# Performance work log

Hardware: AMD Instinct MI355X
Metric: run time of the kernel (lower is better)

The kernel has to match this reference:

```python
import jax, jax.numpy as jnp
import numpy as np

B, Q, K = 4, 512, 512
QUERY_SIZE = 512
KEY_SIZE = 512
NUM_HIDDENS = 256


def setup_inputs() -> dict:
    key = jax.random.key(0)
    k1, k2, k3, k4, k5 = jax.random.split(key, 5)
    queries = jax.random.normal(k1, (B, Q, 1, QUERY_SIZE), dtype=jnp.float32)
    keys = jax.random.normal(k2, (B, 1, K, KEY_SIZE), dtype=jnp.float32)
    # nn.Linear weights (bias=False); stored as (in, out) for einsum clarity
    W_q = jax.random.normal(k3, (QUERY_SIZE, NUM_HIDDENS), dtype=jnp.float32) * (1.0 / np.sqrt(QUERY_SIZE))
    W_k = jax.random.normal(k4, (KEY_SIZE, NUM_HIDDENS), dtype=jnp.float32) * (1.0 / np.sqrt(KEY_SIZE))
    w_v = jax.random.normal(k5, (NUM_HIDDENS,), dtype=jnp.float32) * (1.0 / np.sqrt(NUM_HIDDENS))
    return {"queries": queries, "keys": keys, "W_q": W_q, "W_k": W_k, "w_v": w_v}


def reference(queries, keys, W_q, W_k, w_v):
    # Project: queries (B,Q,1,Dq) -> (B,Q,1,H); keys (B,1,K,Dk) -> (B,1,K,H)
    q = jnp.einsum('bqod,dh->bqoh', queries, W_q)
    k = jnp.einsum('bokd,dh->bokh', keys, W_k)
    # Broadcast add -> (B,Q,K,H), tanh, reduce hidden via w_v -> (B,Q,K)
    features = jnp.tanh(q + k)
    scores = jnp.einsum('bqkh,h->bqk', features, w_v)
    return scores
```

## Files before the change

### kernel.cpp

```cpp
#include <hip/hip_runtime.h>
#include <hip/hip_bf16.h>

#define HH 256
#define DD 512
#define MM 2048
#define CSCALE 2.8853900817779268f

typedef __bf16 bf16x8 __attribute__((ext_vector_type(8)));
typedef float floatx4 __attribute__((ext_vector_type(4)));

__global__ __launch_bounds__(256) void prep_kernel(
    const float* __restrict__ Wq, const float* __restrict__ Wk,
    const float* __restrict__ wv,
    __bf16* __restrict__ Wt, float* __restrict__ wv2, float* __restrict__ sumWp)
{
  const int bx = blockIdx.x;
  if (bx < 256) {
    const int mat  = bx >> 7;
    const int tile = bx & 127;
    const int kt = tile & 15;
    const int nt = tile >> 4;
    const float* __restrict__ W = mat ? Wk : Wq;
    __bf16* __restrict__ Wo = Wt + (size_t)mat * HH * DD;
    __shared__ float lds[32][33];
    const int i = threadIdx.x >> 5;
    const int j = threadIdx.x & 31;
    const int k0 = kt * 32, n0 = nt * 32;
#pragma unroll
    for (int p = 0; p < 4; ++p)
      lds[i + p * 8][j] = W[(k0 + i + p * 8) * HH + n0 + j];
    __syncthreads();
#pragma unroll
    for (int p = 0; p < 4; ++p) {
      const int n = i + p * 8;
      Wo[(n0 + n) * DD + k0 + j] = (__bf16)(lds[j][n] * CSCALE);
    }
  } else {
    __shared__ float red[256];
    const int t = threadIdx.x;
    float w = wv[t];
    wv2[t] = -2.0f * w;
    red[t] = w;
    __syncthreads();
    for (int s = 128; s > 0; s >>= 1) {
      if (t < s) red[t] += red[t + s];
      __syncthreads();
    }
    if (t == 0) *sumWp = red[0];
  }
}

__global__ __launch_bounds__(256) void proj_kernel(
    const float* __restrict__ queries, const float* __restrict__ keys,
    const __bf16* __restrict__ Wt,
    __bf16* __restrict__ eqp, float* __restrict__ ekp)
{
  const int w    = threadIdx.x >> 6;
  const int lane = threadIdx.x & 63;
  const int quad = lane >> 4;
  const int r    = lane & 15;
  const bool is_k = (blockIdx.z != 0);
  const float* __restrict__ X = is_k ? keys : queries;
  const __bf16* __restrict__ Wb = Wt + (is_k ? (size_t)HH * DD : 0);

  const int m0 = blockIdx.x * 32 + (w >> 1) * 16;
  const int n0 = blockIdx.y * 64 + (w & 1) * 32;

  floatx4 acc0 = {0.f, 0.f, 0.f, 0.f};
  floatx4 acc1 = {0.f, 0.f, 0.f, 0.f};
  const float* arow = X + (size_t)(m0 + r) * DD + quad * 8;
  const __bf16* b0 = Wb + (size_t)(n0 + r) * DD + quad * 8;
  const __bf16* b1 = b0 + 16 * DD;

  for (int kk = 0; kk < DD; kk += 32) {
    float4 a0 = *(const float4*)(arow + kk);
    float4 a1 = *(const float4*)(arow + kk + 4);
    bf16x8 af;
    af[0] = (__bf16)a0.x; af[1] = (__bf16)a0.y;
    af[2] = (__bf16)a0.z; af[3] = (__bf16)a0.w;
    af[4] = (__bf16)a1.x; af[5] = (__bf16)a1.y;
    af[6] = (__bf16)a1.z; af[7] = (__bf16)a1.w;
    bf16x8 bf0 = *(const bf16x8*)(b0 + kk);
    bf16x8 bf1 = *(const bf16x8*)(b1 + kk);
    acc0 = __builtin_amdgcn_mfma_f32_16x16x32_bf16(af, bf0, acc0, 0, 0, 0);
    acc1 = __builtin_amdgcn_mfma_f32_16x16x32_bf16(af, bf1, acc1, 0, 0, 0);
  }

  const int mrow = m0 + quad * 4;
  if (!is_k) {
#pragma unroll
    for (int i = 0; i < 4; ++i) {
      eqp[(size_t)(mrow + i) * HH + n0 + r] =
          (__bf16)__builtin_amdgcn_exp2f(acc0[i]);
      eqp[(size_t)(mrow + i) * HH + n0 + 16 + r] =
          (__bf16)__builtin_amdgcn_exp2f(acc1[i]);
    }
  } else {
#pragma unroll
    for (int i = 0; i < 4; ++i) {
      int na = n0 + r, nb = n0 + 16 + r;
      ekp[((size_t)(na >> 2) * MM + (mrow + i)) * 4 + (na & 3)] =
          __builtin_amdgcn_exp2f(acc0[i]);
      ekp[((size_t)(nb >> 2) * MM + (mrow + i)) * 4 + (nb & 3)] =
          __builtin_amdgcn_exp2f(acc1[i]);
    }
  }
}

__global__ __launch_bounds__(256) void score_kernel(
    const __bf16* __restrict__ eqp, const float4* __restrict__ ekp,
    const float* __restrict__ wv2, const float* __restrict__ sumWp,
    float* __restrict__ out)
{
  const int t  = threadIdx.x;
  const int b  = blockIdx.z;
  const int k  = blockIdx.x * 256 + t;
  const int q0 = blockIdx.y * 2;
  const float sumW = *sumWp;

  const float4* __restrict__ kptr = ekp + (size_t)b * 512 + k;
  const unsigned* __restrict__ qrow0 =
      (const unsigned*)(eqp + (size_t)(b * 512 + q0) * HH);
  const unsigned* __restrict__ qrow1 =
      (const unsigned*)(eqp + (size_t)(b * 512 + q0 + 1) * HH);

  float acc0 = 0.f, acc1 = 0.f;

#pragma unroll 8
  for (int hq = 0; hq < 64; ++hq) {
    float4 ek = kptr[(size_t)hq * MM];
    float4 w4 = *(const float4*)(wv2 + hq * 4);
    unsigned pa0 = qrow0[hq * 2], pb0 = qrow0[hq * 2 + 1];
    unsigned pa1 = qrow1[hq * 2], pb1 = qrow1[hq * 2 + 1];
    float q00 = __uint_as_float(pa0 << 16);
    float q01 = __uint_as_float(pa0 & 0xffff0000u);
    float q02 = __uint_as_float(pb0 << 16);
    float q03 = __uint_as_float(pb0 & 0xffff0000u);
    float q10 = __uint_as_float(pa1 << 16);
    float q11 = __uint_as_float(pa1 & 0xffff0000u);
    float q12 = __uint_as_float(pb1 << 16);
    float q13 = __uint_as_float(pb1 & 0xffff0000u);
    acc0 = fmaf(w4.x, __builtin_amdgcn_rcpf(fmaf(q00, ek.x, 1.0f)), acc0);
    acc0 = fmaf(w4.y, __builtin_amdgcn_rcpf(fmaf(q01, ek.y, 1.0f)), acc0);
    acc0 = fmaf(w4.z, __builtin_amdgcn_rcpf(fmaf(q02, ek.z, 1.0f)), acc0);
    acc0 = fmaf(w4.w, __builtin_amdgcn_rcpf(fmaf(q03, ek.w, 1.0f)), acc0);
    acc1 = fmaf(w4.x, __builtin_amdgcn_rcpf(fmaf(q10, ek.x, 1.0f)), acc1);
    acc1 = fmaf(w4.y, __builtin_amdgcn_rcpf(fmaf(q11, ek.y, 1.0f)), acc1);
    acc1 = fmaf(w4.z, __builtin_amdgcn_rcpf(fmaf(q12, ek.z, 1.0f)), acc1);
    acc1 = fmaf(w4.w, __builtin_amdgcn_rcpf(fmaf(q13, ek.w, 1.0f)), acc1);
  }

  const size_t obase = ((size_t)b * 512 + q0) * 512 + blockIdx.x * 256 + t;
  out[obase]       = sumW + acc0;
  out[obase + 512] = sumW + acc1;
}

extern "C" void kernel_launch(void* const* d_in, const int* in_sizes, int n_in,
                              void* d_out, int out_size, void* d_ws, size_t ws_size,
                              hipStream_t stream) {
  (void)in_sizes; (void)n_in; (void)out_size; (void)ws_size;
  const float* queries = (const float*)d_in[0];
  const float* keys    = (const float*)d_in[1];
  const float* Wq      = (const float*)d_in[2];
  const float* Wk      = (const float*)d_in[3];
  const float* wv      = (const float*)d_in[4];
  float* out = (float*)d_out;

  char* ws = (char*)d_ws;
  __bf16* Wt    = (__bf16*)ws;
  float*  wv2   = (float*)(ws + (512 << 10));
  float*  sumWp = (float*)(ws + (513 << 10));
  __bf16* eqp   = (__bf16*)(ws + (1 << 20));
  float*  ekp   = (float*)(ws + (2 << 20));

  prep_kernel<<<dim3(257), 256, 0, stream>>>(Wq, Wk, wv, Wt, wv2, sumWp);
  proj_kernel<<<dim3(64, 4, 2), 256, 0, stream>>>(queries, keys, Wt, eqp, ekp);
  score_kernel<<<dim3(2, 256, 4), 256, 0, stream>>>(
      eqp, (const float4*)ekp, wv2, sumWp, out);
}
```

Baseline: 115.5 us.

## Pair reciprocals in score loop, split-K projection, pre-convert inputs to bf16

The score kernel now merges two reciprocal terms into one, using w0/u0 + w2/u2 = (w0*u2 + w2*u0)/(u0*u2). This halves the rcp instructions per hidden pair. Each block now handles 4 query rows instead of 2, and the exp(q) values are stored as fp32 instead of bf16. The projection GEMM splits K across warps with an LDS reduction and doubles the grid over N. The input fp32-to-bf16 conversion moves into the prep kernel, which costs an extra pass over memory and a larger workspace. The merged reciprocal risks overflow or precision loss when the product of the two u terms gets large.

```diff
diff --git a/kernel.cpp b/kernel.cpp
--- a/kernel.cpp
+++ b/kernel.cpp
@@ -12,7 +12,9 @@
 __global__ __launch_bounds__(256) void prep_kernel(
     const float* __restrict__ Wq, const float* __restrict__ Wk,
     const float* __restrict__ wv,
-    __bf16* __restrict__ Wt, float* __restrict__ wv2, float* __restrict__ sumWp)
+    const float* __restrict__ queries, const float* __restrict__ keys,
+    __bf16* __restrict__ Wt, __bf16* __restrict__ Xbf,
+    float* __restrict__ wv2, float* __restrict__ sumWp)
 {
   const int bx = blockIdx.x;
   if (bx < 256) {
@@ -35,7 +37,7 @@
       const int n = i + p * 8;
       Wo[(n0 + n) * DD + k0 + j] = (__bf16)(lds[j][n] * CSCALE);
     }
-  } else {
+  } else if (bx == 256) {
     __shared__ float red[256];
     const int t = threadIdx.x;
     float w = wv[t];
@@ -47,112 +49,132 @@
       __syncthreads();
     }
     if (t == 0) *sumWp = red[0];
-  }
-}
-
-__global__ __launch_bounds__(256) void proj_kernel(
-    const float* __restrict__ queries, const float* __restrict__ keys,
-    const __bf16* __restrict__ Wt,
-    __bf16* __restrict__ eqp, float* __restrict__ ekp)
+  } else {
+    const int blk = bx - 257;
+    const size_t dst = (size_t)blk * 2048 + threadIdx.x * 8;
+    const float* __restrict__ src =
+        (blk < 512) ? (queries + dst) : (keys + dst - (size_t)1048576);
+    float4 a = *(const float4*)(src);
+    float4 b = *(const float4*)(src + 4);
+    bf16x8 v;
+    v[0] = (__bf16)a.x; v[1] = (__bf16)a.y; v[2] = (__bf16)a.z; v[3] = (__bf16)a.w;
+    v[4] = (__bf16)b.x; v[5] = (__bf16)b.y; v[6] = (__bf16)b.z; v[7] = (__bf16)b.w;
+    *(bf16x8*)(Xbf + dst) = v;
+  }
+}
+
+__global__ __launch_bounds__(256, 4) void proj_kernel(
+    const __bf16* __restrict__ Xbf, const __bf16* __restrict__ Wt,
+    float* __restrict__ eqp, float* __restrict__ ekp)
 {
   const int w    = threadIdx.x >> 6;
   const int lane = threadIdx.x & 63;
   const int quad = lane >> 4;
   const int r    = lane & 15;
+  const int tw = w & 1;
+  const int ks = w >> 1;
   const bool is_k = (blockIdx.z != 0);
-  const float* __restrict__ X = is_k ? keys : queries;
+  const __bf16* __restrict__ X  = Xbf + (is_k ? (size_t)1048576 : 0);
   const __bf16* __restrict__ Wb = Wt + (is_k ? (size_t)HH * DD : 0);
 
-  const int m0 = blockIdx.x * 32 + (w >> 1) * 16;
-  const int n0 = blockIdx.y * 64 + (w & 1) * 32;
+  const int m0 = blockIdx.x * 32 + tw * 16;
+  const int n0 = blockIdx.y * 32;
 
   floatx4 acc0 = {0.f, 0.f, 0.f, 0.f};
   floatx4 acc1 = {0.f, 0.f, 0.f, 0.f};
-  const float* arow = X + (size_t)(m0 + r) * DD + quad * 8;
-  const __bf16* b0 = Wb + (size_t)(n0 + r) * DD + quad * 8;
-  const __bf16* b1 = b0 + 16 * DD;
-
-  for (int kk = 0; kk < DD; kk += 32) {
-    float4 a0 = *(const float4*)(arow + kk);
-    float4 a1 = *(const float4*)(arow + kk + 4);
-    bf16x8 af;
-    af[0] = (__bf16)a0.x; af[1] = (__bf16)a0.y;
-    af[2] = (__bf16)a0.z; af[3] = (__bf16)a0.w;
-    af[4] = (__bf16)a1.x; af[5] = (__bf16)a1.y;
-    af[6] = (__bf16)a1.z; af[7] = (__bf16)a1.w;
+  const __bf16* arow = X + (size_t)(m0 + r) * DD + ks * 256 + quad * 8;
+  const __bf16* b0   = Wb + (size_t)(n0 + r) * DD + ks * 256 + quad * 8;
+  const __bf16* b1   = b0 + 16 * DD;
+
+#pragma unroll
+  for (int kk = 0; kk < 256; kk += 32) {
+    bf16x8 af  = *(const bf16x8*)(arow + kk);
     bf16x8 bf0 = *(const bf16x8*)(b0 + kk);
     bf16x8 bf1 = *(const bf16x8*)(b1 + kk);
     acc0 = __builtin_amdgcn_mfma_f32_16x16x32_bf16(af, bf0, acc0, 0, 0, 0);
     acc1 = __builtin_amdgcn_mfma_f32_16x16x32_bf16(af, bf1, acc1, 0, 0, 0);
   }
 
-  const int mrow = m0 + quad * 4;
-  if (!is_k) {
+  __shared__ float part[2][64][9];
+  if (ks == 1) {
 #pragma unroll
     for (int i = 0; i < 4; ++i) {
-      eqp[(size_t)(mrow + i) * HH + n0 + r] =
-          (__bf16)__builtin_amdgcn_exp2f(acc0[i]);
-      eqp[(size_t)(mrow + i) * HH + n0 + 16 + r] =
-          (__bf16)__builtin_amdgcn_exp2f(acc1[i]);
-    }
-  } else {
+      part[tw][lane][i]     = acc0[i];
+      part[tw][lane][4 + i] = acc1[i];
+    }
+  }
+  __syncthreads();
+  if (ks == 0) {
 #pragma unroll
     for (int i = 0; i < 4; ++i) {
-      int na = n0 + r, nb = n0 + 16 + r;
-      ekp[((size_t)(na >> 2) * MM + (mrow + i)) * 4 + (na & 3)] =
-          __builtin_amdgcn_exp2f(acc0[i]);
-      ekp[((size_t)(nb >> 2) * MM + (mrow + i)) * 4 + (nb & 3)] =
-          __builtin_amdgcn_exp2f(acc1[i]);
-    }
-  }
-}
-
-__global__ __launch_bounds__(256) void score_kernel(
-    const __bf16* __restrict__ eqp, const float4* __restrict__ ekp,
+      acc0[i] += part[tw][lane][i];
+      acc1[i] += part[tw][lane][4 + i];
+    }
+    const int mrow = m0 + quad * 4;
+    if (!is_k) {
+#pragma unroll
+      for (int i = 0; i < 4; ++i) {
+        eqp[(size_t)(mrow + i) * HH + n0 + r] =
+            __builtin_amdgcn_exp2f(acc0[i]);
+        eqp[(size_t)(mrow + i) * HH + n0 + 16 + r] =
+            __builtin_amdgcn_exp2f(acc1[i]);
+      }
+    } else {
+      const int na = n0 + r, nb = n0 + 16 + r;
+#pragma unroll
+      for (int i = 0; i < 4; ++i) {
+        ekp[((size_t)(na >> 2) * MM + (mrow + i)) * 4 + (na & 3)] =
+            __builtin_amdgcn_exp2f(acc0[i]);
+        ekp[((size_t)(nb >> 2) * MM + (mrow + i)) * 4 + (nb & 3)] =
+            __builtin_amdgcn_exp2f(acc1[i]);
+      }
+    }
+  }
+}
+
+__global__ __launch_bounds__(256, 4) void score_kernel(
+    const float* __restrict__ eqp, const float4* __restrict__ ekp,
     const float* __restrict__ wv2, const float* __restrict__ sumWp,
     float* __restrict__ out)
 {
   const int t  = threadIdx.x;
   const int b  = blockIdx.z;
   const int k  = blockIdx.x * 256 + t;
-  const int q0 = blockIdx.y * 2;
+  const int q0 = blockIdx.y * 4;
   const float sumW = *sumWp;
 
   const float4* __restrict__ kptr = ekp + (size_t)b * 512 + k;
-  const unsigned* __restrict__ qrow0 =
-      (const unsigned*)(eqp + (size_t)(b * 512 + q0) * HH);
-  const unsigned* __restrict__ qrow1 =
-      (const unsigned*)(eqp + (size_t)(b * 512 + q0 + 1) * HH);
-
-  float acc0 = 0.f, acc1 = 0.f;
-
-#pragma unroll 8
+  const float* __restrict__ qb = eqp + (size_t)(b * 512 + q0) * HH;
+
+  float acc[4] = {0.f, 0.f, 0.f, 0.f};
+
+#pragma unroll 4
   for (int hq = 0; hq < 64; ++hq) {
-    float4 ek = kptr[(size_t)hq * MM];
-    float4 w4 = *(const float4*)(wv2 + hq * 4);
-    unsigned pa0 = qrow0[hq * 2], pb0 = qrow0[hq * 2 + 1];
-    unsigned pa1 = qrow1[hq * 2], pb1 = qrow1[hq * 2 + 1];
-    float q00 = __uint_as_float(pa0 << 16);
-    float q01 = __uint_as_float(pa0 & 0xffff0000u);
-    float q02 = __uint_as_float(pb0 << 16);
-    float q03 = __uint_as_float(pb0 & 0xffff0000u);
-    float q10 = __uint_as_float(pa1 << 16);
-    float q11 = __uint_as_float(pa1 & 0xffff0000u);
-    float q12 = __uint_as_float(pb1 << 16);
-    float q13 = __uint_as_float(pb1 & 0xffff0000u);
-    acc0 = fmaf(w4.x, __builtin_amdgcn_rcpf(fmaf(q00, ek.x, 1.0f)), acc0);
-    acc0 = fmaf(w4.y, __builtin_amdgcn_rcpf(fmaf(q01, ek.y, 1.0f)), acc0);
-    acc0 = fmaf(w4.z, __builtin_amdgcn_rcpf(fmaf(q02, ek.z, 1.0f)), acc0);
-    acc0 = fmaf(w4.w, __builtin_amdgcn_rcpf(fmaf(q03, ek.w, 1.0f)), acc0);
-    acc1 = fmaf(w4.x, __builtin_amdgcn_rcpf(fmaf(q10, ek.x, 1.0f)), acc1);
-    acc1 = fmaf(w4.y, __builtin_amdgcn_rcpf(fmaf(q11, ek.y, 1.0f)), acc1);
-    acc1 = fmaf(w4.z, __builtin_amdgcn_rcpf(fmaf(q12, ek.z, 1.0f)), acc1);
-    acc1 = fmaf(w4.w, __builtin_amdgcn_rcpf(fmaf(q13, ek.w, 1.0f)), acc1);
-  }
-
-  const size_t obase = ((size_t)b * 512 + q0) * 512 + blockIdx.x * 256 + t;
-  out[obase]       = sumW + acc0;
-  out[obase + 512] = sumW + acc1;
+    float4 ek4 = kptr[(size_t)hq * MM];
+    const float* wq = wv2 + hq * 4;
+    float w0 = wq[0], w1 = wq[1], w2 = wq[2], w3 = wq[3];
+#pragma unroll
+    for (int qi = 0; qi < 4; ++qi) {
+      const float* eqr = qb + qi * HH + hq * 4;
+      float e0 = eqr[0], e1 = eqr[1], e2 = eqr[2], e3 = eqr[3];
+      float u0 = fmaf(e0, ek4.x, 1.0f);
+      float u1 = fmaf(e1, ek4.y, 1.0f);
+      float u2 = fmaf(e2, ek4.z, 1.0f);
+      float u3 = fmaf(e3, ek4.w, 1.0f);
+      float n02 = fmaf(w2, u0, w0 * u2);
+      float n13 = fmaf(w3, u1, w1 * u3);
+      float r02 = __builtin_amdgcn_rcpf(u0 * u2);
+      float r13 = __builtin_amdgcn_rcpf(u1 * u3);
+      acc[qi] = fmaf(n02, r02, acc[qi]);
+      acc[qi] = fmaf(n13, r13, acc[qi]);
+    }
+  }
+
+  const size_t ob = ((size_t)(b * 512 + q0)) * 512 + blockIdx.x * 256 + t;
+  out[ob]        = sumW + acc[0];
+  out[ob + 512]  = sumW + acc[1];
+  out[ob + 1024] = sumW + acc[2];
+  out[ob + 1536] = sumW + acc[3];
 }
 
 extern "C" void kernel_launch(void* const* d_in, const int* in_sizes, int n_in,
@@ -160,7 +182,7 @@
                               hipStream_t stream) {
   (void)in_sizes; (void)n_in; (void)out_size; (void)ws_size;
   const float* queries = (const float*)d_in[0];
-  const float* keys    = (const float*)d_in[1];
+  const float* Keys    = (const float*)d_in[1];
   const float* Wq      = (const float*)d_in[2];
   const float* Wk      = (const float*)d_in[3];
   const float* wv      = (const float*)d_in[4];
@@ -170,11 +192,13 @@
   __bf16* Wt    = (__bf16*)ws;
   float*  wv2   = (float*)(ws + (512 << 10));
   float*  sumWp = (float*)(ws + (513 << 10));
-  __bf16* eqp   = (__bf16*)(ws + (1 << 20));
-  float*  ekp   = (float*)(ws + (2 << 20));
-
-  prep_kernel<<<dim3(257), 256, 0, stream>>>(Wq, Wk, wv, Wt, wv2, sumWp);
-  proj_kernel<<<dim3(64, 4, 2), 256, 0, stream>>>(queries, keys, Wt, eqp, ekp);
-  score_kernel<<<dim3(2, 256, 4), 256, 0, stream>>>(
+  __bf16* Xbf   = (__bf16*)(ws + (1 << 20));
+  float*  eqp   = (float*)(ws + (5ull << 20));
+  float*  ekp   = (float*)(ws + (7ull << 20));
+
+  prep_kernel<<<dim3(1281), 256, 0, stream>>>(
+      Wq, Wk, wv, queries, Keys, Wt, Xbf, wv2, sumWp);
+  proj_kernel<<<dim3(64, 8, 2), 256, 0, stream>>>(Xbf, Wt, eqp, ekp);
+  score_kernel<<<dim3(2, 128, 4), 256, 0, stream>>>(
       eqp, (const float4*)ekp, wv2, sumWp, out);
 }
```

New measurement: 118.2 us. +2.4%, slower.
